# Kernel optimization log

Measured on AMD Instinct MI355X. Metric: run time of the kernel, lower is better.

Reference implementation:

```python
import jax, jax.numpy as jnp
import numpy as np

EPS = 1e-5
NEG_INF = -1e38


def q_shift(x, H, W, gamma=0.25, s=1):
    # x: (B, T, C) with T = H*W. Four channel groups shifted by 1 pixel in +W,-W,+H,-H.
    B, T, C = x.shape
    g = int(C * gamma)
    x4 = x.reshape(B, H, W, C)
    o0 = jnp.pad(x4[..., 0:g], ((0, 0), (0, 0), (s, 0), (0, 0)))[:, :, :W, :]      # shift right along W
    o1 = jnp.pad(x4[..., g:2 * g], ((0, 0), (0, 0), (0, s), (0, 0)))[:, :, s:, :]  # shift left along W
    o2 = jnp.pad(x4[..., 2 * g:3 * g], ((0, 0), (s, 0), (0, 0), (0, 0)))[:, :H, :, :]  # shift down along H
    o3 = jnp.pad(x4[..., 3 * g:4 * g], ((0, 0), (0, s), (0, 0), (0, 0)))[:, s:, :, :]  # shift up along H
    parts = [o0, o1, o2, o3]
    if 4 * g < C:
        parts.append(jnp.zeros((B, H, W, C - 4 * g), x.dtype))
    return jnp.concatenate(parts, axis=-1).reshape(B, T, C)


def wkv(w, u, k, v):
    # Numerically-stable RWKV WKV recurrence.
    # w,u: (C,); k,v: (B,T,C) -> y: (B,T,C)
    B, T, C = k.shape

    def step(carry, kv):
        a, b, p = carry
        kt, vt = kv
        ww = u + kt
        p2 = jnp.maximum(p, ww)
        e1 = jnp.exp(p - p2)
        e2 = jnp.exp(ww - p2)
        y = (e1 * a + e2 * vt) / (e1 * b + e2)
        ww2 = p + w
        p3 = jnp.maximum(ww2, kt)
        f1 = jnp.exp(ww2 - p3)
        f2 = jnp.exp(kt - p3)
        return (f1 * a + f2 * vt, f1 * b + f2, p3), y

    init = (jnp.zeros((B, C), k.dtype), jnp.zeros((B, C), k.dtype),
            jnp.full((B, C), NEG_INF, k.dtype))
    kT = jnp.swapaxes(k, 0, 1)
    vT = jnp.swapaxes(v, 0, 1)
    _, ys = jax.lax.scan(step, init, (kT, vT))
    return jnp.swapaxes(ys, 0, 1)


def layer_norm(x, g, b):
    m = jnp.mean(x, axis=-1, keepdims=True)
    v = jnp.mean(jnp.square(x - m), axis=-1, keepdims=True)
    return (x - m) * jax.lax.rsqrt(v + EPS) * g + b


def setup_inputs() -> dict:
    key = jax.random.key(0)
    ks = jax.random.split(key, 16)
    B, H, W, C = 8, 64, 64, 768
    T = H * W
    sc = 1.0 / np.sqrt(C)
    inp = {
        "x": jax.random.normal(ks[0], (B, T, C), jnp.float32),
        "spatial_decay": jax.random.normal(ks[1], (C,), jnp.float32) * 0.1,
        "spatial_first": jax.random.normal(ks[2], (C,), jnp.float32) * 0.1,
        "mix_k": jax.random.uniform(ks[3], (1, 1, C), jnp.float32),
        "mix_v": jax.random.uniform(ks[4], (1, 1, C), jnp.float32),
        "mix_r": jax.random.uniform(ks[5], (1, 1, C), jnp.float32),
        "Wk": jax.random.normal(ks[6], (C, C), jnp.float32) * sc,
        "Wv": jax.random.normal(ks[7], (C, C), jnp.float32) * sc,
        "Wr": jax.random.normal(ks[8], (C, C), jnp.float32) * sc,
        "Wo": jax.random.normal(ks[9], (C, C), jnp.float32) * sc,
        "ln_g": jnp.ones((C,), jnp.float32),
        "ln_b": jnp.zeros((C,), jnp.float32),
        "Wd1": jax.random.normal(ks[10], (C, C // 4), jnp.float32) * sc,
        "bd1": jnp.zeros((C // 4,), jnp.float32),
        "Wd2": jax.random.normal(ks[11], (C // 4, C), jnp.float32) * (2.0 / np.sqrt(C)),
        "bd2": jnp.full((C,), -3.0, jnp.float32),
        "H": H,
        "W": W,
    }
    return inp


def reference(x, spatial_decay, spatial_first, mix_k, mix_v, mix_r,
              Wk, Wv, Wr, Wo, ln_g, ln_b, Wd1, bd1, Wd2, bd2, H, W):
    B, T, C = x.shape
    xx = q_shift(x, H, W)
    xk = x * mix_k + xx * (1.0 - mix_k)
    xv = x * mix_v + xx * (1.0 - mix_v)
    xr = x * mix_r + xx * (1.0 - mix_r)
    k = xk @ Wk
    v = xv @ Wv
    sr = jax.nn.sigmoid(xr @ Wr)
    # frequency-adaptive decay modulation from global context
    gctx = jnp.mean(x, axis=1)                       # (B, C)
    h = jnp.tanh(gctx @ Wd1 + bd1)                   # (B, C/4)
    mod = jax.nn.sigmoid(h @ Wd2 + bd2)              # (B, C)
    w = spatial_decay + jnp.mean(mod, axis=0)        # (C,)
    y = wkv(w, spatial_first, k, v)                  # (B, T, C)
    y = layer_norm(y, ln_g, ln_b)
    return (sr * y) @ Wo
```

## Files before the change

### kernel.cpp

```cpp
#include <hip/hip_runtime.h>
#include <hip/hip_bf16.h>

typedef __hip_bfloat16 bf16;
typedef short short8 __attribute__((ext_vector_type(8)));
typedef float f32x4 __attribute__((ext_vector_type(4)));

#define T_SEQ 4096
#define HH 64
#define WW2 64
#define C_DIM 768
#define CQ 192
#define LCH 32
#define NCH (T_SEQ / LCH)
#define NCG (C_DIM / 8)
#define TCH 16

__device__ __forceinline__ float b2f(bf16 h) { return __bfloat162float(h); }
__device__ __forceinline__ bf16 f2b(float f) { return __float2bfloat16(f); }
__device__ __forceinline__ float sigmoid_stable(float m) {
  float e = __expf(-fabsf(m));
  return (m >= 0.f) ? 1.f / (1.f + e) : e / (1.f + e);
}

union V16 { uint4 u; bf16 h[8]; };

__global__ void k_detect(const unsigned* __restrict__ p, int* __restrict__ flag) {
  if (threadIdx.x == 0 && blockIdx.x == 0)
    *flag = ((p[0] & 0xFFFFu) == 0u) ? 1 : 0;
}

__global__ void k_convert_b(const void* __restrict__ src, bf16* __restrict__ dst,
                            int n, const int* __restrict__ flag) {
  int i = blockIdx.x * blockDim.x + threadIdx.x;
  if (i >= n) return;
  dst[i] = (*flag) ? f2b(((const float*)src)[i]) : ((const bf16*)src)[i];
}

__global__ void k_convert_small(
    const void* s0, const void* s1, const void* s2, const void* s3, const void* s4,
    const void* s5, const void* s6, const void* s7, const void* s8,
    float* d0, float* d1, float* d2, float* d3, float* d4,
    float* d5, float* d6, float* d7, float* d8, const int* __restrict__ flag) {
  const void* srcs[9] = {s0, s1, s2, s3, s4, s5, s6, s7, s8};
  float* dsts[9] = {d0, d1, d2, d3, d4, d5, d6, d7, d8};
  int a = blockIdx.x;
  int n = (a == 8) ? CQ : C_DIM;
  const void* s = srcs[a];
  float* d = dsts[a];
  bool f32 = (*flag != 0);
  for (int i = threadIdx.x; i < n; i += 256)
    d[i] = f32 ? ((const float*)s)[i] : b2f(((const bf16*)s)[i]);
}

__global__ void k_transpose_d(const void* __restrict__ src, bf16* __restrict__ dst,
                              const int* __restrict__ flag) {
  __shared__ bf16 tile[32][33];
  bool f32 = (*flag != 0);
  int bx = blockIdx.x * 32, by = blockIdx.y * 32;
  int tx = threadIdx.x, ty = threadIdx.y;
  for (int j = ty; j < 32; j += 8) {
    size_t idx = (size_t)(by + j) * C_DIM + bx + tx;
    tile[j][tx] = f32 ? f2b(((const float*)src)[idx]) : ((const bf16*)src)[idx];
  }
  __syncthreads();
  for (int j = ty; j < 32; j += 8)
    dst[(size_t)(bx + j) * C_DIM + by + tx] = tile[tx][j];
}

__global__ void k_shift_mix1(const void* __restrict__ xsrc,
                             const float* __restrict__ mix,
                             bf16* __restrict__ dst, int BT,
                             const int* __restrict__ flag) {
  int idx = blockIdx.x * blockDim.x + threadIdx.x;
  if (idx >= BT * (C_DIM / 8)) return;
  bool f32 = (*flag != 0);
  int c8 = (idx % (C_DIM / 8)) * 8;
  int tg = idx / (C_DIM / 8);
  int t = tg & (T_SEQ - 1);
  int hh = t >> 6, ww = t & (WW2 - 1);
  int g = c8 / CQ;
  int d; bool valid;
  if (g == 0)      { valid = (ww >= 1);        d = -1;   }
  else if (g == 1) { valid = (ww <= WW2 - 2);  d = 1;    }
  else if (g == 2) { valid = (hh >= 1);        d = -WW2; }
  else             { valid = (hh <= HH - 2);   d = WW2;  }
  ptrdiff_t base = (ptrdiff_t)tg * C_DIM + c8;
  float fx[8], fxx[8];
  if (f32) {
    const float* xp = (const float*)xsrc;
#pragma unroll
    for (int i = 0; i < 8; i++) fx[i] = xp[base + i];
    if (valid) {
#pragma unroll
      for (int i = 0; i < 8; i++) fxx[i] = xp[base + (ptrdiff_t)d * C_DIM + i];
    } else {
#pragma unroll
      for (int i = 0; i < 8; i++) fxx[i] = 0.f;
    }
  } else {
    const bf16* xp = (const bf16*)xsrc;
    V16 xin; xin.u = *(const uint4*)(xp + base);
    V16 xxv;
    if (valid) xxv.u = *(const uint4*)(xp + base + (ptrdiff_t)d * C_DIM);
    else       xxv.u = make_uint4(0u, 0u, 0u, 0u);
#pragma unroll
    for (int i = 0; i < 8; i++) { fx[i] = b2f(xin.h[i]); fxx[i] = b2f(xxv.h[i]); }
  }
  V16 o;
#pragma unroll
  for (int i = 0; i < 8; i++)
    o.h[i] = f2b(fxx[i] + mix[c8 + i] * (fx[i] - fxx[i]));
  *(uint4*)(dst + base) = o.u;
}

__global__ __launch_bounds__(256) void k_shift_mix3(
    const void* __restrict__ xsrc,
    const float* __restrict__ mk, const float* __restrict__ mv, const float* __restrict__ mr,
    bf16* __restrict__ xk, bf16* __restrict__ xv, bf16* __restrict__ xr,
    float* __restrict__ gpart, const int* __restrict__ flag) {
  __shared__ float sh[C_DIM];
  int tid = threadIdx.x;
  sh[tid] = 0.f; sh[tid + 256] = 0.f; sh[tid + 512] = 0.f;
  __syncthreads();
  int gid = blockIdx.x * 256 + tid;
  bool f32 = (*flag != 0);
  int cg = gid % NCG;
  int tc = gid / NCG;
  int c0 = cg * 8;
  int b = tc / (T_SEQ / TCH);
  int t0 = (tc % (T_SEQ / TCH)) * TCH;
  int g = c0 / CQ;
  float mkv[8], mvv[8], mrv[8];
#pragma unroll
  for (int i = 0; i < 8; i++) { mkv[i] = mk[c0 + i]; mvv[i] = mv[c0 + i]; mrv[i] = mr[c0 + i]; }
  float gs[8];
#pragma unroll
  for (int i = 0; i < 8; i++) gs[i] = 0.f;
  for (int tt = 0; tt < TCH; tt++) {
    int t = t0 + tt;
    int hh = t >> 6, ww = t & (WW2 - 1);
    int d; bool valid;
    if (g == 0)      { valid = (ww >= 1);        d = -1;   }
    else if (g == 1) { valid = (ww <= WW2 - 2);  d = 1;    }
    else if (g == 2) { valid = (hh >= 1);        d = -WW2; }
    else             { valid = (hh <= HH - 2);   d = WW2;  }
    ptrdiff_t base = ((ptrdiff_t)b * T_SEQ + t) * C_DIM + c0;
    float fx[8], fxx[8];
    if (f32) {
      const float* xp = (const float*)xsrc;
      float4 a0 = *(const float4*)(xp + base);
      float4 a1 = *(const float4*)(xp + base + 4);
      fx[0] = a0.x; fx[1] = a0.y; fx[2] = a0.z; fx[3] = a0.w;
      fx[4] = a1.x; fx[5] = a1.y; fx[6] = a1.z; fx[7] = a1.w;
      if (valid) {
        float4 b0 = *(const float4*)(xp + base + (ptrdiff_t)d * C_DIM);
        float4 b1 = *(const float4*)(xp + base + (ptrdiff_t)d * C_DIM + 4);
        fxx[0] = b0.x; fxx[1] = b0.y; fxx[2] = b0.z; fxx[3] = b0.w;
        fxx[4] = b1.x; fxx[5] = b1.y; fxx[6] = b1.z; fxx[7] = b1.w;
      } else {
#pragma unroll
        for (int i = 0; i < 8; i++) fxx[i] = 0.f;
      }
    } else {
      const bf16* xp = (const bf16*)xsrc;
      V16 xin; xin.u = *(const uint4*)(xp + base);
      V16 xxv;
      if (valid) xxv.u = *(const uint4*)(xp + base + (ptrdiff_t)d * C_DIM);
      else       xxv.u = make_uint4(0u, 0u, 0u, 0u);
#pragma unroll
      for (int i = 0; i < 8; i++) { fx[i] = b2f(xin.h[i]); fxx[i] = b2f(xxv.h[i]); }
    }
    V16 ok, ov, orr;
#pragma unroll
    for (int i = 0; i < 8; i++) {
      gs[i] += fx[i];
      ok.h[i]  = f2b(fxx[i] + mkv[i] * (fx[i] - fxx[i]));
      ov.h[i]  = f2b(fxx[i] + mvv[i] * (fx[i] - fxx[i]));
      orr.h[i] = f2b(fxx[i] + mrv[i] * (fx[i] - fxx[i]));
    }
    *(uint4*)(xk + base) = ok.u;
    *(uint4*)(xv + base) = ov.u;
    *(uint4*)(xr + base) = orr.u;
  }
#pragma unroll
  for (int i = 0; i < 8; i++) atomicAdd(&sh[c0 + i], gs[i]);
  __syncthreads();
  float* gp = gpart + (size_t)blockIdx.x * C_DIM;
  gp[tid] = sh[tid]; gp[tid + 256] = sh[tid + 256]; gp[tid + 512] = sh[tid + 512];
}

__global__ void k_gctx_reduce(const float* __restrict__ gpart, float* __restrict__ gctx,
                              int B, int blk_per_b) {
  int idx = blockIdx.x * 256 + threadIdx.x;
  if (idx >= B * C_DIM) return;
  int b = idx / C_DIM, c = idx % C_DIM;
  const float* pp = gpart + (size_t)b * blk_per_b * C_DIM + c;
  float s = 0.f;
  for (int j = 0; j < blk_per_b; j++) s += pp[(size_t)j * C_DIM];
  gctx[idx] = s;
}

__global__ void k_gctx(const void* __restrict__ xsrc, float* __restrict__ gctx,
                       const int* __restrict__ flag) {
  bool f32 = (*flag != 0);
  int c = threadIdx.x;
  int chunk = blockIdx.x;
  int b = blockIdx.y;
  size_t base = ((size_t)b * T_SEQ + (size_t)chunk * 128) * C_DIM + c;
  float s = 0.f;
  if (f32) {
    const float* p = (const float*)xsrc;
    for (int t = 0; t < 128; t++) s += p[base + (size_t)t * C_DIM];
  } else {
    const bf16* p = (const bf16*)xsrc;
    for (int t = 0; t < 128; t++) s += b2f(p[base + (size_t)t * C_DIM]);
  }
  atomicAdd(&gctx[b * C_DIM + c], s);
}

__global__ void k_mod(const float* __restrict__ gctx,
                      const bf16* __restrict__ Wd1, const float* __restrict__ bd1,
                      const bf16* __restrict__ Wd2, const float* __restrict__ bd2,
                      float* __restrict__ wsum, int B) {
  __shared__ float hsh[CQ];
  int b = blockIdx.x, j = threadIdx.x;
  const float invT = 1.0f / (float)T_SEQ;
  float acc = bd1[j];
  for (int i = 0; i < C_DIM; i++)
    acc += (gctx[b * C_DIM + i] * invT) * b2f(Wd1[(size_t)i * CQ + j]);
  hsh[j] = tanhf(acc);
  __syncthreads();
  float invB = 1.0f / (float)B;
  for (int cc = j; cc < C_DIM; cc += CQ) {
    float m = bd2[cc];
    for (int jj = 0; jj < CQ; jj++)
      m += hsh[jj] * b2f(Wd2[(size_t)jj * C_DIM + cc]);
    atomicAdd(&wsum[cc], sigmoid_stable(m) * invB);
  }
}

__device__ __forceinline__ void g2l16(const void* g, void* s) {
  __builtin_amdgcn_global_load_lds(
      (const __attribute__((address_space(1))) unsigned int*)g,
      (__attribute__((address_space(3))) unsigned int*)s, 16, 0, 0);
}

template <int MODE>
__global__ __launch_bounds__(256) void k_gemm_bt(
    const bf16* __restrict__ A, const bf16* __restrict__ Bt, void* __restrict__ Cout,
    const bf16* __restrict__ Y, const float* __restrict__ stats,
    const float* __restrict__ lng, const float* __restrict__ lnb,
    const int* __restrict__ flag) {
  const int K = C_DIM, N = C_DIM;
  __shared__ __align__(16) char smem[32768];
  bf16* sA = (bf16*)smem;
  bf16* sB = (bf16*)(smem + 8192);
  int tid = threadIdx.x;
  int wv = tid >> 6, lane = tid & 63;
  int lm = lane & 15, quad = lane >> 4;
  int n0 = blockIdx.x * 128, m0 = blockIdx.y * 128;
  int wm = (wv & 1) * 64, wn = (wv >> 1) * 64;

  f32x4 acc[4][4];
#pragma unroll
  for (int i = 0; i < 4; i++)
#pragma unroll
    for (int j = 0; j < 4; j++) acc[i][j] = f32x4{0.f, 0.f, 0.f, 0.f};

  const bf16* Abase = A + (size_t)m0 * K;
  const bf16* Bbase = Bt + (size_t)n0 * K;
  int ci0 = wv * 128 + lane;
  int ci1 = wv * 128 + 64 + lane;

  for (int kc = 0; kc < K; kc += 32) {
    g2l16(Abase + (size_t)(ci0 >> 2) * K + kc + (ci0 & 3) * 8, (char*)sA + (size_t)(wv * 128) * 16);
    g2l16(Abase + (size_t)(ci1 >> 2) * K + kc + (ci1 & 3) * 8, (char*)sA + (size_t)(wv * 128 + 64) * 16);
    g2l16(Bbase + (size_t)(ci0 >> 2) * K + kc + (ci0 & 3) * 8, (char*)sB + (size_t)(wv * 128) * 16);
    g2l16(Bbase + (size_t)(ci1 >> 2) * K + kc + (ci1 & 3) * 8, (char*)sB + (size_t)(wv * 128 + 64) * 16);
    __syncthreads();
    short8 af[4], bfr[4];
#pragma unroll
    for (int i = 0; i < 4; i++)
      af[i] = *(const short8*)(sA + (size_t)(wm + i * 16 + lm) * 32 + quad * 8);
#pragma unroll
    for (int j = 0; j < 4; j++)
      bfr[j] = *(const short8*)(sB + (size_t)(wn + j * 16 + lm) * 32 + quad * 8);
#pragma unroll
    for (int i = 0; i < 4; i++)
#pragma unroll
      for (int j = 0; j < 4; j++)
        acc[i][j] = __builtin_amdgcn_mfma_f32_16x16x32_bf16(af[i], bfr[j], acc[i][j], 0, 0, 0);
    __syncthreads();
  }

  bool f32out = (MODE == 2) && (*flag != 0);
  if (!f32out) {
    bf16* sC = (bf16*)smem;
#pragma unroll
    for (int i = 0; i < 4; i++)
#pragma unroll
      for (int j = 0; j < 4; j++)
#pragma unroll
        for (int r = 0; r < 4; r++) {
          int m = wm + i * 16 + quad * 4 + r;
          int n = wn + j * 16 + lm;
          float v = acc[i][j][r];
          if (MODE == 1 || MODE == 3) v = sigmoid_stable(v);
          sC[m * 128 + n] = f2b(v);
        }
    __syncthreads();
    int c16 = tid & 15, r0 = tid >> 4;
#pragma unroll
    for (int it = 0; it < 8; it++) {
      int r = r0 + it * 16;
      V16 val; val.u = *(const uint4*)(sC + r * 128 + c16 * 8);
      size_t gbase = (size_t)(m0 + r) * N + n0 + c16 * 8;
      if (MODE == 3) {
        float mu = stats[2 * (m0 + r)], rs = stats[2 * (m0 + r) + 1];
        V16 yv; yv.u = *(const uint4*)(Y + gbase);
        const float* lg = lng + n0 + c16 * 8;
        const float* lb = lnb + n0 + c16 * 8;
        V16 o;
#pragma unroll
        for (int jj = 0; jj < 8; jj++)
          o.h[jj] = f2b(b2f(val.h[jj]) * ((b2f(yv.h[jj]) - mu) * rs * lg[jj] + lb[jj]));
        *(uint4*)((bf16*)Cout + gbase) = o.u;
      } else {
        *(uint4*)((bf16*)Cout + gbase) = val.u;
      }
    }
  } else {
    float* sCf = (float*)smem;
#pragma unroll
    for (int half = 0; half < 2; half++) {
      if (half) __syncthreads();
      if ((wv & 1) == half) {
#pragma unroll
        for (int i = 0; i < 4; i++)
#pragma unroll
          for (int j = 0; j < 4; j++)
#pragma unroll
            for (int r = 0; r < 4; r++) {
              int mrow = i * 16 + quad * 4 + r;
              int n = wn + j * 16 + lm;
              sCf[mrow * 128 + n] = acc[i][j][r];
            }
      }
      __syncthreads();
      int c32 = tid & 31, r0 = tid >> 5;
#pragma unroll
      for (int it = 0; it < 8; it++) {
        int r = r0 + it * 8;
        float4 val = *(const float4*)(sCf + r * 128 + c32 * 4);
        *(float4*)((float*)Cout + (size_t)(m0 + half * 64 + r) * N + n0 + c32 * 4) = val;
      }
    }
  }
}

__device__ __forceinline__ void wkv_acc_step(const V16& kv, const V16& vv,
    const float* __restrict__ w, float* a, float* bb, float* p) {
#pragma unroll
  for (int i = 0; i < 8; i++) {
    float kt = b2f(kv.h[i]), vt = b2f(vv.h[i]);
    float ww2 = p[i] + w[i];
    float p3 = fmaxf(ww2, kt);
    float f1 = __expf(ww2 - p3);
    float f2 = __expf(kt - p3);
    a[i] = f1 * a[i] + f2 * vt;
    bb[i] = f1 * bb[i] + f2;
    p[i] = p3;
  }
}

__device__ __forceinline__ void wkv_out_step(const V16& kv, const V16& vv,
    const float* __restrict__ w, const float* __restrict__ u,
    float* aa, float* bb, float* pp, V16& o) {
#pragma unroll
  for (int i = 0; i < 8; i++) {
    float kt = b2f(kv.h[i]), vt = b2f(vv.h[i]);
    float ww = u[i] + kt;
    float p2 = fmaxf(pp[i], ww);
    float e1 = __expf(pp[i] - p2);
    float e2 = __expf(ww - p2);
    o.h[i] = f2b((e1 * aa[i] + e2 * vt) / (e1 * bb[i] + e2));
    float ww2 = pp[i] + w[i];
    float p3 = fmaxf(ww2, kt);
    float f1 = __expf(ww2 - p3);
    float f2 = __expf(kt - p3);
    aa[i] = f1 * aa[i] + f2 * vt;
    bb[i] = f1 * bb[i] + f2;
    pp[i] = p3;
  }
}

__global__ __launch_bounds__(256) void k_wkv_p1(
    const bf16* __restrict__ kb, const bf16* __restrict__ vb,
    const float* __restrict__ sd, const float* __restrict__ wsum,
    float* __restrict__ ca, float* __restrict__ cb, float* __restrict__ cp, int B) {
  int gid = blockIdx.x * 256 + threadIdx.x;
  if (gid >= B * NCH * NCG) return;
  int cg = gid % NCG;
  int ch = (gid / NCG) % NCH;
  int b  = gid / (NCG * NCH);
  int c0 = cg * 8;
  float w[8], a[8], bbv[8], p[8];
#pragma unroll
  for (int i = 0; i < 8; i++) {
    w[i] = sd[c0 + i] + wsum[c0 + i];
    a[i] = 0.f; bbv[i] = 0.f; p[i] = -1e38f;
  }
  const bf16* kp = kb + ((size_t)b * T_SEQ + (size_t)ch * LCH) * C_DIM + c0;
  const bf16* vp = vb + ((size_t)b * T_SEQ + (size_t)ch * LCH) * C_DIM + c0;
  V16 k0, k1, k2, k3, v0, v1, v2, v3;
  k0.u = *(const uint4*)(kp);              v0.u = *(const uint4*)(vp);
  k1.u = *(const uint4*)(kp + C_DIM);      v1.u = *(const uint4*)(vp + C_DIM);
  k2.u = *(const uint4*)(kp + 2 * C_DIM);  v2.u = *(const uint4*)(vp + 2 * C_DIM);
  k3.u = *(const uint4*)(kp + 3 * C_DIM);  v3.u = *(const uint4*)(vp + 3 * C_DIM);
  for (int t = 0; t + 4 < LCH; t += 4) {
    wkv_acc_step(k0, v0, w, a, bbv, p);
    k0.u = *(const uint4*)(kp + (size_t)(t + 4) * C_DIM); v0.u = *(const uint4*)(vp + (size_t)(t + 4) * C_DIM);
    wkv_acc_step(k1, v1, w, a, bbv, p);
    k1.u = *(const uint4*)(kp + (size_t)(t + 5) * C_DIM); v1.u = *(const uint4*)(vp + (size_t)(t + 5) * C_DIM);
    wkv_acc_step(k2, v2, w, a, bbv, p);
    k2.u = *(const uint4*)(kp + (size_t)(t + 6) * C_DIM); v2.u = *(const uint4*)(vp + (size_t)(t + 6) * C_DIM);
    wkv_acc_step(k3, v3, w, a, bbv, p);
    k3.u = *(const uint4*)(kp + (size_t)(t + 7) * C_DIM); v3.u = *(const uint4*)(vp + (size_t)(t + 7) * C_DIM);
  }
  wkv_acc_step(k0, v0, w, a, bbv, p);
  wkv_acc_step(k1, v1, w, a, bbv, p);
  wkv_acc_step(k2, v2, w, a, bbv, p);
  wkv_acc_step(k3, v3, w, a, bbv, p);
  size_t so = ((size_t)b * NCH + ch) * C_DIM + c0;
#pragma unroll
  for (int i = 0; i < 8; i++) { ca[so + i] = a[i]; cb[so + i] = bbv[i]; cp[so + i] = p[i]; }
}

__global__ void k_wkv_p2(float* __restrict__ ca, float* __restrict__ cb,
                         float* __restrict__ cp,
                         const float* __restrict__ sd, const float* __restrict__ wsum,
                         int B) {
  int tid = blockIdx.x * blockDim.x + threadIdx.x;
  if (tid >= B * C_DIM) return;
  int b = tid / C_DIM, c = tid % C_DIM;
  float wL = (sd[c] + wsum[c]) * (float)LCH;
  float a = 0.f, bb = 0.f, p = -1e38f;
  for (int base = 0; base < NCH; base += 16) {
    float la[16], lb[16], lp[16];
#pragma unroll
    for (int j = 0; j < 16; j++) {
      size_t idx = ((size_t)b * NCH + base + j) * C_DIM + c;
      la[j] = ca[idx]; lb[j] = cb[idx]; lp[j] = cp[idx];
    }
#pragma unroll
    for (int j = 0; j < 16; j++) {
      size_t idx = ((size_t)b * NCH + base + j) * C_DIM + c;
      ca[idx] = a; cb[idx] = bb; cp[idx] = p;
      float pw = p + wL;
      float pn = fmaxf(pw, lp[j]);
      float e1 = __expf(pw - pn);
      float e2 = __expf(lp[j] - pn);
      a = e1 * a + e2 * la[j];
      bb = e1 * bb + e2 * lb[j];
      p = pn;
    }
  }
}

__global__ __launch_bounds__(256) void k_wkv_p3(
    const bf16* __restrict__ kb, const bf16* __restrict__ vb,
    const float* __restrict__ sd, const float* __restrict__ sf,
    const float* __restrict__ wsum,
    const float* __restrict__ ca, const float* __restrict__ cb,
    const float* __restrict__ cp, bf16* __restrict__ y, int B) {
  int gid = blockIdx.x * 256 + threadIdx.x;
  if (gid >= B * NCH * NCG) return;
  int cg = gid % NCG;
  int ch = (gid / NCG) % NCH;
  int b  = gid / (NCG * NCH);
  int c0 = cg * 8;
  size_t so = ((size_t)b * NCH + ch) * C_DIM + c0;
  float w[8], u[8], aa[8], bbv[8], pp[8];
#pragma unroll
  for (int i = 0; i < 8; i++) {
    w[i] = sd[c0 + i] + wsum[c0 + i];
    u[i] = sf[c0 + i];
    aa[i] = ca[so + i]; bbv[i] = cb[so + i]; pp[i] = cp[so + i];
  }
  const bf16* kp = kb + ((size_t)b * T_SEQ + (size_t)ch * LCH) * C_DIM + c0;
  const bf16* vp = vb + ((size_t)b * T_SEQ + (size_t)ch * LCH) * C_DIM + c0;
  bf16* yp = y + ((size_t)b * T_SEQ + (size_t)ch * LCH) * C_DIM + c0;
  V16 k0, k1, k2, k3, v0, v1, v2, v3, o;
  k0.u = *(const uint4*)(kp);              v0.u = *(const uint4*)(vp);
  k1.u = *(const uint4*)(kp + C_DIM);      v1.u = *(const uint4*)(vp + C_DIM);
  k2.u = *(const uint4*)(kp + 2 * C_DIM);  v2.u = *(const uint4*)(vp + 2 * C_DIM);
  k3.u = *(const uint4*)(kp + 3 * C_DIM);  v3.u = *(const uint4*)(vp + 3 * C_DIM);
  for (int t = 0; t + 4 < LCH; t += 4) {
    wkv_out_step(k0, v0, w, u, aa, bbv, pp, o);
    *(uint4*)(yp + (size_t)t * C_DIM) = o.u;
    k0.u = *(const uint4*)(kp + (size_t)(t + 4) * C_DIM); v0.u = *(const uint4*)(vp + (size_t)(t + 4) * C_DIM);
    wkv_out_step(k1, v1, w, u, aa, bbv, pp, o);
    *(uint4*)(yp + (size_t)(t + 1) * C_DIM) = o.u;
    k1.u = *(const uint4*)(kp + (size_t)(t + 5) * C_DIM); v1.u = *(const uint4*)(vp + (size_t)(t + 5) * C_DIM);
    wkv_out_step(k2, v2, w, u, aa, bbv, pp, o);
    *(uint4*)(yp + (size_t)(t + 2) * C_DIM) = o.u;
    k2.u = *(const uint4*)(kp + (size_t)(t + 6) * C_DIM); v2.u = *(const uint4*)(vp + (size_t)(t + 6) * C_DIM);
    wkv_out_step(k3, v3, w, u, aa, bbv, pp, o);
    *(uint4*)(yp + (size_t)(t + 3) * C_DIM) = o.u;
    k3.u = *(const uint4*)(kp + (size_t)(t + 7) * C_DIM); v3.u = *(const uint4*)(vp + (size_t)(t + 7) * C_DIM);
  }
  wkv_out_step(k0, v0, w, u, aa, bbv, pp, o);
  *(uint4*)(yp + (size_t)(LCH - 4) * C_DIM) = o.u;
  wkv_out_step(k1, v1, w, u, aa, bbv, pp, o);
  *(uint4*)(yp + (size_t)(LCH - 3) * C_DIM) = o.u;
  wkv_out_step(k2, v2, w, u, aa, bbv, pp, o);
  *(uint4*)(yp + (size_t)(LCH - 2) * C_DIM) = o.u;
  wkv_out_step(k3, v3, w, u, aa, bbv, pp, o);
  *(uint4*)(yp + (size_t)(LCH - 1) * C_DIM) = o.u;
}

__global__ __launch_bounds__(256) void k_ln_stats(const bf16* __restrict__ y,
                                                  float* __restrict__ stats) {
  int row = blockIdx.x;
  int tid = threadIdx.x;
  const bf16* yr = y + (size_t)row * C_DIM;
  float v0 = b2f(yr[tid]), v1 = b2f(yr[tid + 256]), v2 = b2f(yr[tid + 512]);
  float s1 = v0 + v1 + v2;
  float s2 = v0 * v0 + v1 * v1 + v2 * v2;
#pragma unroll
  for (int off = 32; off >= 1; off >>= 1) {
    s1 += __shfl_xor(s1, off, 64);
    s2 += __shfl_xor(s2, off, 64);
  }
  __shared__ float sh1[4], sh2[4];
  int wv = tid >> 6, lane = tid & 63;
  if (lane == 0) { sh1[wv] = s1; sh2[wv] = s2; }
  __syncthreads();
  if (tid == 0) {
    float t1 = sh1[0] + sh1[1] + sh1[2] + sh1[3];
    float t2 = sh2[0] + sh2[1] + sh2[2] + sh2[3];
    float mean = t1 * (1.f / (float)C_DIM);
    float var = t2 * (1.f / (float)C_DIM) - mean * mean;
    stats[2 * row] = mean;
    stats[2 * row + 1] = rsqrtf(var + 1e-5f);
  }
}

extern "C" void kernel_launch(void* const* d_in, const int* in_sizes, int n_in,
                              void* d_out, int out_size, void* d_ws, size_t ws_size,
                              hipStream_t stream) {
  const void* x   = d_in[0];
  const void* sd  = d_in[1];
  const void* sf  = d_in[2];
  const void* mk  = d_in[3];
  const void* mv  = d_in[4];
  const void* mr  = d_in[5];
  const void* Wk  = d_in[6];
  const void* Wv  = d_in[7];
  const void* Wr  = d_in[8];
  const void* Wo  = d_in[9];
  const void* lng = d_in[10];
  const void* lnb = d_in[11];
  const void* Wd1 = d_in[12];
  const void* bd1 = d_in[13];
  const void* Wd2 = d_in[14];
  const void* bd2 = d_in[15];

  const int C = in_sizes[1];
  const int BT = in_sizes[0] / C;
  const int B = BT / T_SEQ;

  const size_t S  = (size_t)BT * C * sizeof(bf16);
  const size_t WB = (size_t)C * C * sizeof(bf16);
  const size_t WD = (size_t)C * CQ * sizeof(bf16);
  const size_t CS = (size_t)B * NCH * C * sizeof(float);
  const int nblk_mix = (BT / TCH) * NCG / 256;
  const int blk_per_b = nblk_mix / B;
  const size_t GP = (size_t)nblk_mix * C * sizeof(float);
  const size_t rest = 4 * WB + 2 * WD + ((size_t)8 * C + CQ + (size_t)B * C + C) * 4
                      + 16 + 15 + 3 * CS + (size_t)BT * 8 + GP + 256;
  const bool fused = (ws_size >= 3 * S + rest);

  char* p = (char*)d_ws;
  bf16* slot0 = (bf16*)p; p += S;
  bf16* slot1 = (bf16*)p; p += S;
  bf16* slot2 = nullptr;
  if (fused) { slot2 = (bf16*)p; p += S; }
  bf16* WkT = (bf16*)p; p += WB;
  bf16* WvT = (bf16*)p; p += WB;
  bf16* WrT = (bf16*)p; p += WB;
  bf16* WoT = (bf16*)p; p += WB;
  bf16* Wd1c = (bf16*)p; p += WD;
  bf16* Wd2c = (bf16*)p; p += WD;
  float* sd_f  = (float*)p; p += C * 4;
  float* sf_f  = (float*)p; p += C * 4;
  float* mk_f  = (float*)p; p += C * 4;
  float* mv_f  = (float*)p; p += C * 4;
  float* mr_f  = (float*)p; p += C * 4;
  float* lng_f = (float*)p; p += C * 4;
  float* lnb_f = (float*)p; p += C * 4;
  float* bd2_f = (float*)p; p += C * 4;
  float* bd1_f = (float*)p; p += CQ * 4;
  float* gctx  = (float*)p; p += (size_t)B * C * 4;
  float* wsum  = (float*)p; p += C * 4;
  int* flag    = (int*)p; p += 16;
  p = (char*)(((uintptr_t)p + 15) & ~(uintptr_t)15);
  float* ca = (float*)p; p += CS;
  float* cb = (float*)p; p += CS;
  float* cp = (float*)p; p += CS;
  float* stats = (float*)p; p += (size_t)BT * 8;
  float* gpart = (float*)p; p += GP;

  bf16* stage = (bf16*)d_out;

  k_detect<<<1, 64, 0, stream>>>((const unsigned*)lng, flag);
  hipMemsetAsync(gctx, 0, (size_t)(B * C + C) * sizeof(float), stream);

  k_convert_small<<<9, 256, 0, stream>>>(sd, sf, mk, mv, mr, lng, lnb, bd2, bd1,
                                         sd_f, sf_f, mk_f, mv_f, mr_f, lng_f, lnb_f,
                                         bd2_f, bd1_f, flag);
  k_convert_b<<<(C * CQ + 255) / 256, 256, 0, stream>>>(Wd1, Wd1c, C * CQ, flag);
  k_convert_b<<<(C * CQ + 255) / 256, 256, 0, stream>>>(Wd2, Wd2c, C * CQ, flag);

  dim3 tb(32, 8), tg(C / 32, C / 32);
  k_transpose_d<<<tg, tb, 0, stream>>>(Wk, WkT, flag);
  k_transpose_d<<<tg, tb, 0, stream>>>(Wv, WvT, flag);
  k_transpose_d<<<tg, tb, 0, stream>>>(Wr, WrT, flag);
  k_transpose_d<<<tg, tb, 0, stream>>>(Wo, WoT, flag);

  dim3 gg(C / 128, BT / 128);
  int scan_threads = B * NCH * NCG;
  int scan_blocks = (scan_threads + 255) / 256;

  if (fused) {
    k_shift_mix3<<<nblk_mix, 256, 0, stream>>>(x, mk_f, mv_f, mr_f,
                                               slot0, stage, slot1, gpart, flag);
    k_gctx_reduce<<<(B * C + 255) / 256, 256, 0, stream>>>(gpart, gctx, B, blk_per_b);
    k_mod<<<B, CQ, 0, stream>>>(gctx, Wd1c, bd1_f, Wd2c, bd2_f, wsum, B);

    k_gemm_bt<0><<<gg, 256, 0, stream>>>(slot0, WkT, slot2, nullptr, nullptr, nullptr, nullptr, flag);
    k_gemm_bt<0><<<gg, 256, 0, stream>>>(stage, WvT, slot0, nullptr, nullptr, nullptr, nullptr, flag);

    k_wkv_p1<<<scan_blocks, 256, 0, stream>>>(slot2, slot0, sd_f, wsum, ca, cb, cp, B);
    k_wkv_p2<<<(B * C + 255) / 256, 256, 0, stream>>>(ca, cb, cp, sd_f, wsum, B);
    k_wkv_p3<<<scan_blocks, 256, 0, stream>>>(slot2, slot0, sd_f, sf_f, wsum, ca, cb, cp, stage, B);

    k_ln_stats<<<BT, 256, 0, stream>>>(stage, stats);
    k_gemm_bt<3><<<gg, 256, 0, stream>>>(slot1, WrT, slot0, stage, stats, lng_f, lnb_f, flag);
    k_gemm_bt<2><<<gg, 256, 0, stream>>>(slot0, WoT, d_out, nullptr, nullptr, nullptr, nullptr, flag);
  } else {
    int nthr = BT * (C / 8);
    int nblk = (nthr + 255) / 256;
    k_gctx<<<dim3(32, B), C, 0, stream>>>(x, gctx, flag);
    k_mod<<<B, CQ, 0, stream>>>(gctx, Wd1c, bd1_f, Wd2c, bd2_f, wsum, B);

    k_shift_mix1<<<nblk, 256, 0, stream>>>(x, mk_f, stage, BT, flag);
    k_gemm_bt<0><<<gg, 256, 0, stream>>>(stage, WkT, slot0, nullptr, nullptr, nullptr, nullptr, flag);
    k_shift_mix1<<<nblk, 256, 0, stream>>>(x, mv_f, stage, BT, flag);
    k_gemm_bt<0><<<gg, 256, 0, stream>>>(stage, WvT, slot1, nullptr, nullptr, nullptr, nullptr, flag);

    k_wkv_p1<<<scan_blocks, 256, 0, stream>>>(slot0, slot1, sd_f, wsum, ca, cb, cp, B);
    k_wkv_p2<<<(B * C + 255) / 256, 256, 0, stream>>>(ca, cb, cp, sd_f, wsum, B);
    k_wkv_p3<<<scan_blocks, 256, 0, stream>>>(slot0, slot1, sd_f, sf_f, wsum, ca, cb, cp, stage, B);

    k_ln_stats<<<BT, 256, 0, stream>>>(stage, stats);
    k_shift_mix1<<<nblk, 256, 0, stream>>>(x, mr_f, slot0, BT, flag);
    k_gemm_bt<3><<<gg, 256, 0, stream>>>(slot0, WrT, slot1, stage, stats, lng_f, lnb_f, flag);
    k_gemm_bt<2><<<gg, 256, 0, stream>>>(slot1, WoT, d_out, nullptr, nullptr, nullptr, nullptr, flag);
  }
}
```

Before: 707.9 us.

## Double-buffer GEMM LDS tiles, swizzle LDS layout, remap blocks per XCD

The bf16 MFMA GEMM now double-buffers its shared-memory tiles, so the global-to-LDS loads for the next K-slice are issued before the current slice is consumed. Each iteration keeps a single barrier instead of two. Loads use an XOR swizzle on the 16-byte chunk index to reduce LDS bank conflicts on the fragment reads. The grid becomes 1D with a remap that gives each XCD a contiguous range of tiles, for better L2 reuse of A and B. In exchange the kernel uses all 32KB of LDS, and it relies on the async global_load_lds writes and the single barrier being ordered correctly.

Result: faster. 676.3 us (-4.5%).

```diff
diff --git a/kernel.cpp b/kernel.cpp
--- a/kernel.cpp
+++ b/kernel.cpp
@@ -250,15 +250,21 @@
     const bf16* __restrict__ A, const bf16* __restrict__ Bt, void* __restrict__ Cout,
     const bf16* __restrict__ Y, const float* __restrict__ stats,
     const float* __restrict__ lng, const float* __restrict__ lnb,
-    const int* __restrict__ flag) {
+    const int* __restrict__ flag, int nmb) {
   const int K = C_DIM, N = C_DIM;
+  const int NNB = C_DIM / 128;
   __shared__ __align__(16) char smem[32768];
-  bf16* sA = (bf16*)smem;
-  bf16* sB = (bf16*)(smem + 8192);
   int tid = threadIdx.x;
   int wv = tid >> 6, lane = tid & 63;
   int lm = lane & 15, quad = lane >> 4;
-  int n0 = blockIdx.x * 128, m0 = blockIdx.y * 128;
+
+  int nwg = nmb * NNB;
+  int orig = blockIdx.x;
+  int xcd = orig & 7;
+  int q8 = nwg >> 3, r8 = nwg & 7;
+  int lin = (xcd < r8) ? (xcd * (q8 + 1) + (orig >> 3))
+                       : (r8 * (q8 + 1) + (xcd - r8) * q8 + (orig >> 3));
+  int m0 = (lin / NNB) * 128, n0 = (lin % NNB) * 128;
   int wm = (wv & 1) * 64, wn = (wv >> 1) * 64;
 
   f32x4 acc[4][4];
@@ -271,26 +277,48 @@
   const bf16* Bbase = Bt + (size_t)n0 * K;
   int ci0 = wv * 128 + lane;
   int ci1 = wv * 128 + 64 + lane;
-
-  for (int kc = 0; kc < K; kc += 32) {
-    g2l16(Abase + (size_t)(ci0 >> 2) * K + kc + (ci0 & 3) * 8, (char*)sA + (size_t)(wv * 128) * 16);
-    g2l16(Abase + (size_t)(ci1 >> 2) * K + kc + (ci1 & 3) * 8, (char*)sA + (size_t)(wv * 128 + 64) * 16);
-    g2l16(Bbase + (size_t)(ci0 >> 2) * K + kc + (ci0 & 3) * 8, (char*)sB + (size_t)(wv * 128) * 16);
-    g2l16(Bbase + (size_t)(ci1 >> 2) * K + kc + (ci1 & 3) * 8, (char*)sB + (size_t)(wv * 128 + 64) * 16);
-    __syncthreads();
+  int r0 = ci0 >> 2, r1 = ci1 >> 2;
+  size_t off0 = (size_t)r0 * K + (size_t)(((ci0 & 3) ^ (r0 & 3)) * 8);
+  size_t off1 = (size_t)r1 * K + (size_t)(((ci1 & 3) ^ (r1 & 3)) * 8);
+  char* dstA0 = smem + wv * 2048;
+  char* dstA1 = smem + wv * 2048 + 1024;
+  char* dstB0 = smem + 16384 + wv * 2048;
+  char* dstB1 = smem + 16384 + wv * 2048 + 1024;
+
+  const int NT = K / 32;
+  g2l16(Abase + off0, dstA0);
+  g2l16(Abase + off1, dstA1);
+  g2l16(Bbase + off0, dstB0);
+  g2l16(Bbase + off1, dstB1);
+  __syncthreads();
+
+  int cur = 0;
+  int swz = (lm & 3);
+  for (int t = 0; t < NT; ++t) {
+    if (t + 1 < NT) {
+      int kc = (t + 1) * 32;
+      int nb = (cur ^ 1) * 8192;
+      g2l16(Abase + off0 + kc, dstA0 + nb);
+      g2l16(Abase + off1 + kc, dstA1 + nb);
+      g2l16(Bbase + off0 + kc, dstB0 + nb);
+      g2l16(Bbase + off1 + kc, dstB1 + nb);
+    }
+    const bf16* sAr = (const bf16*)(smem + cur * 8192);
+    const bf16* sBr = (const bf16*)(smem + 16384 + cur * 8192);
     short8 af[4], bfr[4];
 #pragma unroll
     for (int i = 0; i < 4; i++)
-      af[i] = *(const short8*)(sA + (size_t)(wm + i * 16 + lm) * 32 + quad * 8);
+      af[i] = *(const short8*)(sAr + (size_t)(wm + i * 16 + lm) * 32 + ((quad ^ swz) * 8));
 #pragma unroll
     for (int j = 0; j < 4; j++)
-      bfr[j] = *(const short8*)(sB + (size_t)(wn + j * 16 + lm) * 32 + quad * 8);
+      bfr[j] = *(const short8*)(sBr + (size_t)(wn + j * 16 + lm) * 32 + ((quad ^ swz) * 8));
 #pragma unroll
     for (int i = 0; i < 4; i++)
 #pragma unroll
       for (int j = 0; j < 4; j++)
         acc[i][j] = __builtin_amdgcn_mfma_f32_16x16x32_bf16(af[i], bfr[j], acc[i][j], 0, 0, 0);
     __syncthreads();
+    cur ^= 1;
   }
 
   bool f32out = (MODE == 2) && (*flag != 0);
@@ -305,14 +333,14 @@
           int m = wm + i * 16 + quad * 4 + r;
           int n = wn + j * 16 + lm;
           float v = acc[i][j][r];
-          if (MODE == 1 || MODE == 3) v = sigmoid_stable(v);
+          if (MODE == 3) v = sigmoid_stable(v);
           sC[m * 128 + n] = f2b(v);
         }
     __syncthreads();
-    int c16 = tid & 15, r0 = tid >> 4;
+    int c16 = tid & 15, rr0 = tid >> 4;
 #pragma unroll
     for (int it = 0; it < 8; it++) {
-      int r = r0 + it * 16;
+      int r = rr0 + it * 16;
       V16 val; val.u = *(const uint4*)(sC + r * 128 + c16 * 8);
       size_t gbase = (size_t)(m0 + r) * N + n0 + c16 * 8;
       if (MODE == 3) {
@@ -347,10 +375,10 @@
             }
       }
       __syncthreads();
-      int c32 = tid & 31, r0 = tid >> 5;
+      int c32 = tid & 31, rr0 = tid >> 5;
 #pragma unroll
       for (int it = 0; it < 8; it++) {
-        int r = r0 + it * 8;
+        int r = rr0 + it * 8;
         float4 val = *(const float4*)(sCf + r * 128 + c32 * 4);
         *(float4*)((float*)Cout + (size_t)(m0 + half * 64 + r) * N + n0 + c32 * 4) = val;
       }
@@ -628,7 +656,8 @@
   k_transpose_d<<<tg, tb, 0, stream>>>(Wr, WrT, flag);
   k_transpose_d<<<tg, tb, 0, stream>>>(Wo, WoT, flag);
 
-  dim3 gg(C / 128, BT / 128);
+  const int nmb = BT / 128;
+  const int ngemm = nmb * (C / 128);
   int scan_threads = B * NCH * NCG;
   int scan_blocks = (scan_threads + 255) / 256;
 
@@ -638,16 +667,16 @@
     k_gctx_reduce<<<(B * C + 255) / 256, 256, 0, stream>>>(gpart, gctx, B, blk_per_b);
     k_mod<<<B, CQ, 0, stream>>>(gctx, Wd1c, bd1_f, Wd2c, bd2_f, wsum, B);
 
-    k_gemm_bt<0><<<gg, 256, 0, stream>>>(slot0, WkT, slot2, nullptr, nullptr, nullptr, nullptr, flag);
-    k_gemm_bt<0><<<gg, 256, 0, stream>>>(stage, WvT, slot0, nullptr, nullptr, nullptr, nullptr, flag);
+    k_gemm_bt<0><<<ngemm, 256, 0, stream>>>(slot0, WkT, slot2, nullptr, nullptr, nullptr, nullptr, flag, nmb);
+    k_gemm_bt<0><<<ngemm, 256, 0, stream>>>(stage, WvT, slot0, nullptr, nullptr, nullptr, nullptr, flag, nmb);
 
     k_wkv_p1<<<scan_blocks, 256, 0, stream>>>(slot2, slot0, sd_f, wsum, ca, cb, cp, B);
     k_wkv_p2<<<(B * C + 255) / 256, 256, 0, stream>>>(ca, cb, cp, sd_f, wsum, B);
     k_wkv_p3<<<scan_blocks, 256, 0, stream>>>(slot2, slot0, sd_f, sf_f, wsum, ca, cb, cp, stage, B);
 
     k_ln_stats<<<BT, 256, 0, stream>>>(stage, stats);
-    k_gemm_bt<3><<<gg, 256, 0, stream>>>(slot1, WrT, slot0, stage, stats, lng_f, lnb_f, flag);
-    k_gemm_bt<2><<<gg, 256, 0, stream>>>(slot0, WoT, d_out, nullptr, nullptr, nullptr, nullptr, flag);
+    k_gemm_bt<3><<<ngemm, 256, 0, stream>>>(slot1, WrT, slot0, stage, stats, lng_f, lnb_f, flag, nmb);
+    k_gemm_bt<2><<<ngemm, 256, 0, stream>>>(slot0, WoT, d_out, nullptr, nullptr, nullptr, nullptr, flag, nmb);
   } else {
     int nthr = BT * (C / 8);
     int nblk = (nthr + 255) / 256;
@@ -655,9 +684,9 @@
     k_mod<<<B, CQ, 0, stream>>>(gctx, Wd1c, bd1_f, Wd2c, bd2_f, wsum, B);
 
     k_shift_mix1<<<nblk, 256, 0, stream>>>(x, mk_f, stage, BT, flag);
-    k_gemm_bt<0><<<gg, 256, 0, stream>>>(stage, WkT, slot0, nullptr, nullptr, nullptr, nullptr, flag);
+    k_gemm_bt<0><<<ngemm, 256, 0, stream>>>(stage, WkT, slot0, nullptr, nullptr, nullptr, nullptr, flag, nmb);
     k_shift_mix1<<<nblk, 256, 0, stream>>>(x, mv_f, stage, BT, flag);
-    k_gemm_bt<0><<<gg, 256, 0, stream>>>(stage, WvT, slot1, nullptr, nullptr, nullptr, nullptr, flag);
+    k_gemm_bt<0><<<ngemm, 256, 0, stream>>>(stage, WvT, slot1, nullptr, nullptr, nullptr, nullptr, flag, nmb);
 
     k_wkv_p1<<<scan_blocks, 256, 0, stream>>>(slot0, slot1, sd_f, wsum, ca, cb, cp, B);
     k_wkv_p2<<<(B * C + 255) / 256, 256, 0, stream>>>(ca, cb, cp, sd_f, wsum, B);
@@ -665,7 +694,7 @@
 
     k_ln_stats<<<BT, 256, 0, stream>>>(stage, stats);
     k_shift_mix1<<<nblk, 256, 0, stream>>>(x, mr_f, slot0, BT, flag);
-    k_gemm_bt<3><<<gg, 256, 0, stream>>>(slot0, WrT, slot1, stage, stats, lng_f, lnb_f, flag);
-    k_gemm_bt<2><<<gg, 256, 0, stream>>>(slot1, WoT, d_out, nullptr, nullptr, nullptr, nullptr, flag);
-  }
-}
+    k_gemm_bt<3><<<ngemm, 256, 0, stream>>>(slot0, WrT, slot1, stage, stats, lng_f, lnb_f, flag, nmb);
+    k_gemm_bt<2><<<ngemm, 256, 0, stream>>>(slot1, WoT, d_out, nullptr, nullptr, nullptr, nullptr, flag, nmb);
+  }
+}
```
